# Kernel optimization log

Measured on AMD Instinct MI355X. Metric: run time of the kernel, lower is better.

Reference implementation:

```python
import jax, jax.numpy as jnp
import numpy as np

B, G, D, N_HEADS, FFN, L = 16, 2048, 256, 8, 1024, 4
HEAD_DIM = D // N_HEADS
EPS_LN = 1e-5
MASK_TOKEN = -10.0
REE_BASE = 100.0


def setup_inputs() -> dict:
    key = jax.random.key(0)
    ks = jax.random.split(key, 20)
    s = 0.02
    inp = {
        'x': jax.random.normal(ks[0], (B, G), jnp.float32),
        'gene_emb': jax.random.normal(ks[1], (G, D), jnp.float32) * s,
        'inv_freq': (1.0 / REE_BASE ** (jnp.arange(0, D, 2, dtype=jnp.float32) / D)),
        'Wq': jax.random.normal(ks[2], (L, D, D), jnp.float32) * s,
        'bq': jnp.zeros((L, D), jnp.float32),
        'Wk': jax.random.normal(ks[3], (L, D, D), jnp.float32) * s,
        'bk': jnp.zeros((L, D), jnp.float32),
        'Wv': jax.random.normal(ks[4], (L, D, D), jnp.float32) * s,
        'bv': jnp.zeros((L, D), jnp.float32),
        'ln1_g': jnp.ones((L, D), jnp.float32),
        'ln1_b': jnp.zeros((L, D), jnp.float32),
        'ln2_g': jnp.ones((L, D), jnp.float32),
        'ln2_b': jnp.zeros((L, D), jnp.float32),
        'WU': jax.random.normal(ks[5], (L, D, FFN), jnp.float32) * s,
        'bU': jnp.zeros((L, FFN), jnp.float32),
        'WV': jax.random.normal(ks[6], (L, FFN, D), jnp.float32) * s,
        'bV': jnp.zeros((L, D), jnp.float32),
        'Wout': jax.random.normal(ks[7], (D, 1), jnp.float32) * s,
        'bout': jnp.zeros((1,), jnp.float32),
    }
    return inp


def layernorm(x, g, b):
    m = x.mean(-1, keepdims=True)
    v = ((x - m) ** 2).mean(-1, keepdims=True)
    return (x - m) / jnp.sqrt(v + EPS_LN) * g + b


def causal_linear_attention(q, k, v):
    # q, k already feature-mapped ('sqr'); shapes [B, S, H, dh]
    b, s, h, dh = q.shape
    qs, ks_, vs = (jnp.moveaxis(t, 1, 0) for t in (q, k, v))  # [S,B,H,dh]
    num0 = jnp.zeros((b, h, dh, dh), q.dtype)
    den0 = jnp.zeros((b, h, dh), q.dtype)

    def step(carry, qkv):
        num_s, den_s = carry
        qt, kt, vt = qkv
        num_s = num_s + jnp.einsum('bhf,bhd->bhfd', kt, vt)
        den_s = den_s + kt
        num = jnp.einsum('bhf,bhfd->bhd', qt, num_s)
        den = jnp.einsum('bhf,bhf->bh', qt, den_s)
        return (num_s, den_s), num / (den[..., None] + 1e-16)

    _, out = jax.lax.scan(step, (num0, den0), (qs, ks_, vs))  # [S,B,H,dh]
    return jnp.moveaxis(out, 0, 1).reshape(b, s, h * dh)


def reference(x, gene_emb, inv_freq, Wq, bq, Wk, bk, Wv, bv,
              ln1_g, ln1_b, ln2_g, ln2_b, WU, bU, WV, bV, Wout, bout):
    b, g = x.shape
    # Rotary Expression Embedding
    freqs = x[..., None] * inv_freq  # [B,G,D/2]
    emb = jnp.concatenate([jnp.sin(freqs), jnp.cos(freqs)], axis=-1)  # [B,G,D]
    emb = jnp.where((x == MASK_TOKEN)[..., None], 0.0, emb)
    h = gene_emb[None] + emb  # [B,G,D]

    for l in range(Wq.shape[0]):
        hn = layernorm(h, ln1_g[l], ln1_b[l])  # pre-LN (on_gptln=True)
        q = (hn @ Wq[l] + bq[l]).reshape(b, g, N_HEADS, HEAD_DIM) ** 2
        k = (hn @ Wk[l] + bk[l]).reshape(b, g, N_HEADS, HEAD_DIM) ** 2
        v = (hn @ Wv[l] + bv[l]).reshape(b, g, N_HEADS, HEAD_DIM)
        h = h + causal_linear_attention(q, k, v)
        hn2 = layernorm(h, ln2_g[l], ln2_b[l])
        h = h + jax.nn.gelu(hn2 @ WU[l] + bU[l], approximate=False) @ WV[l] + bV[l]
    return (h @ Wout + bout).squeeze(-1)  # [B,G]
```

## Files before the change

kernel.cpp:

```cpp
#include <hip/hip_runtime.h>
#include <math.h>


#define GG 2048
#define DD 256
#define NROWS 32768
#define NC 32
#define CS 64

typedef __attribute__((ext_vector_type(8))) short bf16x8;
typedef __attribute__((ext_vector_type(4))) float f32x4;

struct FalseT { static constexpr bool value = false; };
struct TrueT  { static constexpr bool value = true;  };

__device__ __forceinline__ short f2bf(float f) {
  union { float f; unsigned u; } v; v.f = f;
  unsigned r = v.u + 0x7FFFu + ((v.u >> 16) & 1u);
  return (short)(r >> 16);
}
__device__ __forceinline__ float bf2f(short s) {
  union { unsigned u; float f; } v; v.u = ((unsigned)(unsigned short)s) << 16;
  return v.f;
}
__device__ __forceinline__ void gld16(const short* g, short* l) {
  __builtin_amdgcn_global_load_lds(
      (const __attribute__((address_space(1))) void*)g,
      (__attribute__((address_space(3))) void*)l, 16, 0, 0);
}
__device__ __forceinline__ float fast_gelu(float x) {
  float y = 1.595769122f * (x + 0.044715f * x * x * x);
  return x / (1.0f + __expf(-y));
}

__global__ __launch_bounds__(256) void embed_kernel(
    const float* __restrict__ x, const float* __restrict__ ge,
    const float* __restrict__ invf, float* __restrict__ h) {
  int bg = blockIdx.x * 4 + (threadIdx.x >> 6);
  int g = bg & (GG - 1);
  int lane = threadIdx.x & 63;
  float xv = x[bg];
  int d = lane * 4;
  float4 e;
  if (lane < 32) {
    float4 f = *(const float4*)&invf[d];
    e.x = sinf(xv * f.x); e.y = sinf(xv * f.y);
    e.z = sinf(xv * f.z); e.w = sinf(xv * f.w);
  } else {
    float4 f = *(const float4*)&invf[d - 128];
    e.x = cosf(xv * f.x); e.y = cosf(xv * f.y);
    e.z = cosf(xv * f.z); e.w = cosf(xv * f.w);
  }
  if (xv == -10.0f) { e.x = 0.f; e.y = 0.f; e.z = 0.f; e.w = 0.f; }
  float4 gv = *(const float4*)&ge[(size_t)g * DD + d];
  float4 o; o.x = gv.x + e.x; o.y = gv.y + e.y; o.z = gv.z + e.z; o.w = gv.w + e.w;
  *(float4*)&h[(size_t)bg * DD + d] = o;
}

__global__ __launch_bounds__(256) void ln_tiled(
    const float* __restrict__ h, const float* __restrict__ gamma,
    const float* __restrict__ beta, short* __restrict__ outT) {
  __shared__ float mean_s[32], rstd_s[32];
  __shared__ float gls[256], bls[256];
  int r0 = blockIdx.x * 32;
  int tid = threadIdx.x;
  gls[tid] = gamma[tid]; bls[tid] = beta[tid];
  {
    int row = tid >> 3, seg = tid & 7;
    const float4* hp = (const float4*)(h + (size_t)(r0 + row) * DD + seg * 32);
    float s = 0.f, s2 = 0.f;
#pragma unroll
    for (int i = 0; i < 8; ++i) {
      float4 v = hp[i];
      s += v.x + v.y + v.z + v.w;
      s2 += v.x * v.x + v.y * v.y + v.z * v.z + v.w * v.w;
    }
    s += __shfl_xor(s, 1); s += __shfl_xor(s, 2); s += __shfl_xor(s, 4);
    s2 += __shfl_xor(s2, 1); s2 += __shfl_xor(s2, 2); s2 += __shfl_xor(s2, 4);
    if (seg == 0) {
      float mn = s * (1.0f / 256.0f);
      mean_s[row] = mn;
      rstd_s[row] = rsqrtf(s2 * (1.0f / 256.0f) - mn * mn + 1e-5f);
    }
  }
  __syncthreads();
  int row = tid & 31, kc8 = (tid >> 5) & 3, half = tid >> 7;
  float mn = mean_s[row], rs = rstd_s[row];
  size_t hrow = (size_t)(r0 + row) * DD;
  int trow = (r0 & 127) + row;
  short* tb = outT + (size_t)(r0 >> 7) * 8 * 4096 + (kc8 * 128 + trow) * 8;
#pragma unroll
  for (int j = 0; j < 4; ++j) {
    int kb = half * 4 + j;
    int k0 = kb * 32 + kc8 * 8;
    float4 x0 = *(const float4*)&h[hrow + k0];
    float4 x1 = *(const float4*)&h[hrow + k0 + 4];
    float4 g0 = *(const float4*)&gls[k0], g1 = *(const float4*)&gls[k0 + 4];
    float4 b0 = *(const float4*)&bls[k0], b1 = *(const float4*)&bls[k0 + 4];
    bf16x8 aw;
    aw[0] = f2bf((x0.x - mn) * rs * g0.x + b0.x);
    aw[1] = f2bf((x0.y - mn) * rs * g0.y + b0.y);
    aw[2] = f2bf((x0.z - mn) * rs * g0.z + b0.z);
    aw[3] = f2bf((x0.w - mn) * rs * g0.w + b0.w);
    aw[4] = f2bf((x1.x - mn) * rs * g1.x + b1.x);
    aw[5] = f2bf((x1.y - mn) * rs * g1.y + b1.y);
    aw[6] = f2bf((x1.z - mn) * rs * g1.z + b1.z);
    aw[7] = f2bf((x1.w - mn) * rs * g1.w + b1.w);
    *(bf16x8*)&tb[(size_t)kb * 4096] = aw;
  }
}

__global__ __launch_bounds__(256) void prep_weights(
    const float* __restrict__ Wq, const float* __restrict__ Wk,
    const float* __restrict__ Wv, const float* __restrict__ WU,
    const float* __restrict__ WV,
    short* __restrict__ TQ, short* __restrict__ TK, short* __restrict__ TV,
    short* __restrict__ TU, short* __restrict__ TVd) {
  int zz = blockIdx.z, l = blockIdx.y;
  const float* src; short* dst; int Kd, Nd;
  if (zz == 0) { src = Wq; dst = TQ; Kd = 256; Nd = 256; }
  else if (zz == 1) { src = Wk; dst = TK; Kd = 256; Nd = 256; }
  else if (zz == 2) { src = Wv; dst = TV; Kd = 256; Nd = 256; }
  else if (zz == 3) { src = WU; dst = TU; Kd = 256; Nd = 1024; }
  else { src = WV; dst = TVd; Kd = 1024; Nd = 256; }
  int tot = Kd * Nd;
  int e = blockIdx.x * 256 + threadIdx.x;
  if (e >= tot) return;
  int t = e >> 12;
  int cslot = (e >> 3) & 511;
  int elem = e & 7;
  int kc8 = cslot >> 7, rn = cslot & 127;
  int nKb = Kd >> 5;
  int nt = t / nKb, kb = t - nt * nKb;
  int n = nt * 128 + rn, k = kb * 32 + kc8 * 8 + elem;
  dst[(size_t)l * tot + e] = f2bf(src[(size_t)l * tot + (size_t)k * Nd + n]);
}

template <int K, int EPI>
__global__ __launch_bounds__(256) void gemm_t(
    const short* __restrict__ A, const short* __restrict__ B0,
    const short* __restrict__ B1, const short* __restrict__ B2,
    const float* __restrict__ bias0, const float* __restrict__ bias1,
    const float* __restrict__ bias2,
    short* __restrict__ o0, short* __restrict__ o1, short* __restrict__ o2,
    float* __restrict__ outf, int N) {
  __shared__ __align__(16) short L[24576];
  constexpr int nIter = K / 32;
  int z = blockIdx.z;
  const short* Bt = (z == 0) ? B0 : (z == 1) ? B1 : B2;
  const float* bias = (z == 0) ? bias0 : (z == 1) ? bias1 : bias2;
  short* outz = (z == 0) ? o0 : (z == 1) ? o1 : o2;
  int m0 = blockIdx.x * 128, n0 = blockIdx.y * 128;
  int tid = threadIdx.x;
  int lane = tid & 63, w = tid >> 6;
  int q = lane >> 4, r = lane & 15;
  int wm = (w >> 1) * 64, wn = (w & 1) * 64;
  const short* At = A + (size_t)blockIdx.x * nIter * 4096;
  const short* Btl = Bt + (size_t)blockIdx.y * nIter * 4096;
  f32x4 vzero = {0.f, 0.f, 0.f, 0.f};
  f32x4 acc[4][4];
#pragma unroll
  for (int i = 0; i < 4; ++i)
#pragma unroll
    for (int j = 0; j < 4; ++j) acc[i][j] = vzero;

  int c0 = tid * 8, c1 = (tid + 256) * 8;
#pragma unroll
  for (int g = 0; g < 3; ++g) {
    gld16(At + g * 4096 + c0, &L[g * 4096 + c0]);
    gld16(At + g * 4096 + c1, &L[g * 4096 + c1]);
    gld16(Btl + g * 4096 + c0, &L[12288 + g * 4096 + c0]);
    gld16(Btl + g * 4096 + c1, &L[12288 + g * 4096 + c1]);
  }

  int abase = (q * 128 + wm + r) * 8;
  int bbase = (q * 128 + wn + r) * 8;

#pragma unroll
  for (int gi = 0; gi < nIter; ++gi) {
    const int rem = nIter - 1 - gi;
    if (rem >= 2)      __builtin_amdgcn_s_waitcnt(0x0f78);
    else if (rem == 1) __builtin_amdgcn_s_waitcnt(0x0f74);
    else               __builtin_amdgcn_s_waitcnt(0x0f70);
    __builtin_amdgcn_s_barrier();
    const int cur = gi % 3;
    const short* Asc = &L[cur * 4096];
    const short* Bsc = &L[12288 + cur * 4096];
    bf16x8 af[4], bfr[4];
#pragma unroll
    for (int mt = 0; mt < 4; ++mt)
      af[mt] = *(const bf16x8*)&Asc[abase + mt * 16 * 8];
#pragma unroll
    for (int nt = 0; nt < 4; ++nt)
      bfr[nt] = *(const bf16x8*)&Bsc[bbase + nt * 16 * 8];
#pragma unroll
    for (int mt = 0; mt < 4; ++mt)
#pragma unroll
      for (int nt = 0; nt < 4; ++nt)
        acc[mt][nt] = __builtin_amdgcn_mfma_f32_16x16x32_bf16(bfr[nt], af[mt], acc[mt][nt], 0, 0, 0);
    __builtin_amdgcn_s_waitcnt(0xc07f);
    __builtin_amdgcn_s_barrier();
    if (gi + 3 < nIter) {
      size_t kn = (size_t)(gi + 3) * 4096;
      gld16(At + kn + c0, &L[cur * 4096 + c0]);
      gld16(At + kn + c1, &L[cur * 4096 + c1]);
      gld16(Btl + kn + c0, &L[12288 + cur * 4096 + c0]);
      gld16(Btl + kn + c1, &L[12288 + cur * 4096 + c1]);
    }
  }

  float4 bias4[4];
#pragma unroll
  for (int nt = 0; nt < 4; ++nt) bias4[nt] = *(const float4*)&bias[n0 + wn + nt * 16 + q * 4];

  if (EPI == 0) {
    short* T = L;
#pragma unroll
    for (int mt = 0; mt < 4; ++mt) {
      int ml = wm + mt * 16 + r;
#pragma unroll
      for (int nt = 0; nt < 4; ++nt) {
        f32x4 v = acc[mt][nt];
        v[0] += bias4[nt].x; v[1] += bias4[nt].y; v[2] += bias4[nt].z; v[3] += bias4[nt].w;
        if (z < 2) { v[0] *= v[0]; v[1] *= v[1]; v[2] *= v[2]; v[3] *= v[3]; }
        short4 pk; pk.x = f2bf(v[0]); pk.y = f2bf(v[1]); pk.z = f2bf(v[2]); pk.w = f2bf(v[3]);
        *(short4*)&T[ml * 132 + wn + nt * 16 + q * 4] = pk;
      }
    }
    __syncthreads();
#pragma unroll
    for (int t2 = 0; t2 < 2; ++t2) {
      int task = tid + t2 * 256;
      int row = task & 127, hl = task >> 7;
      size_t obase = ((size_t)((n0 >> 5) + hl) * NROWS + m0 + row) * 32;
#pragma unroll
      for (int j = 0; j < 4; ++j)
        *(bf16x8*)&outz[obase + j * 8] = *(const bf16x8*)&T[row * 132 + hl * 32 + j * 8];
    }
  } else if (EPI == 1) {
#pragma unroll
    for (int mt = 0; mt < 4; ++mt) {
      int ml = wm + mt * 16 + r;
#pragma unroll
      for (int nt = 0; nt < 4; ++nt) {
        f32x4 v = acc[mt][nt];
        v[0] += bias4[nt].x; v[1] += bias4[nt].y; v[2] += bias4[nt].z; v[3] += bias4[nt].w;
#pragma unroll
        for (int e = 0; e < 4; ++e) v[e] = fast_gelu(v[e]);
        short4 o; o.x = f2bf(v[0]); o.y = f2bf(v[1]); o.z = f2bf(v[2]); o.w = f2bf(v[3]);
        int n = n0 + wn + nt * 16 + q * 4;
        size_t ti = ((size_t)blockIdx.x * (N >> 5) + (n >> 5)) * 4096 +
                    (size_t)(((n >> 3) & 3) << 10) + (ml << 3) + (n & 7);
        *(short4*)&outz[ti] = o;
      }
    }
  } else {
    float* TF = (float*)L;
#pragma unroll
    for (int half = 0; half < 2; ++half) {
      __syncthreads();
      if ((w & 1) == half) {
#pragma unroll
        for (int mt = 0; mt < 4; ++mt) {
          int ml = wm + mt * 16 + r;
#pragma unroll
          for (int nt = 0; nt < 4; ++nt) {
            f32x4 v = acc[mt][nt];
            v[0] += bias4[nt].x; v[1] += bias4[nt].y; v[2] += bias4[nt].z; v[3] += bias4[nt].w;
            *(f32x4*)&TF[ml * 68 + nt * 16 + q * 4] = v;
          }
        }
      }
      __syncthreads();
      int row = tid >> 1, col = (tid & 1) * 32;
      size_t hoff = (size_t)(m0 + row) * N + n0 + half * 64 + col;
#pragma unroll
      for (int j = 0; j < 8; ++j) {
        float4 add = *(const float4*)&TF[row * 68 + col + j * 4];
        float4 cur4 = *(float4*)&outf[hoff + j * 4];
        cur4.x += add.x; cur4.y += add.y; cur4.z += add.z; cur4.w += add.w;
        *(float4*)&outf[hoff + j * 4] = cur4;
      }
    }
  }
}

__global__ __launch_bounds__(512) void ffn_fused(
    const short* __restrict__ A, const short* __restrict__ TUw,
    const short* __restrict__ TVw, const float* __restrict__ bUp,
    const float* __restrict__ bVp, float* __restrict__ h) {
  __shared__ __align__(16) short L[75776];
  float* BU = (float*)&L[73728];
  int tid = threadIdx.x;
  int lane = tid & 63, w = tid >> 6;
  int q = lane >> 4, r = lane & 15;
  int wmU = (w >> 2) * 64, wnU = (w & 3) * 32;
  int wmD = (w >> 2) * 64, wnD = (w & 3) * 64;
  int c16 = tid * 8;
  const short* At = A + (size_t)blockIdx.x * 32768;

  if (tid < 256) *(float4*)&BU[tid * 4] = *(const float4*)&bUp[tid * 4];

#pragma unroll
  for (int i = 0; i < 8; ++i) gld16(At + i * 4096 + c16, &L[i * 4096 + c16]);

  auto issueUp = [&](int ss, int jj, int buf) {
    short* dst = &L[49152 + buf * 8192];
    const short* g0 = TUw + ((size_t)ss * 8 + jj * 2) * 4096;
    gld16(g0 + c16, dst + c16);
    gld16(g0 + 4096 + c16, dst + 4096 + c16);
  };
  auto issueDown = [&](int ss, int ii, int buf) {
    short* dst = &L[49152 + buf * 8192];
    gld16(TVw + (size_t)(ss * 4 + ii) * 4096 + c16, dst + c16);
    gld16(TVw + (size_t)(32 + ss * 4 + ii) * 4096 + c16, dst + 4096 + c16);
  };

  issueUp(0, 0, 0); issueUp(0, 1, 1); issueUp(0, 2, 2);

  f32x4 vzero = {0.f, 0.f, 0.f, 0.f};
  f32x4 accm[4][2], acco[4][4];
#pragma unroll
  for (int mt = 0; mt < 4; ++mt) {
#pragma unroll
    for (int nt = 0; nt < 2; ++nt) accm[mt][nt] = vzero;
#pragma unroll
    for (int nt = 0; nt < 4; ++nt) acco[mt][nt] = vzero;
  }

  int cur = 0;

  auto slice = [&](int s, auto lastc) {
    constexpr bool LAST = decltype(lastc)::value;
#pragma unroll
    for (int j = 0; j < 4; ++j) {
      __builtin_amdgcn_s_waitcnt(0x0f74);
      __builtin_amdgcn_s_barrier();
      const short* Ws = &L[49152 + cur * 8192];
#pragma unroll
      for (int kk = 0; kk < 2; ++kk) {
        int kb = j * 2 + kk;
        bf16x8 af[4], bfr[2];
#pragma unroll
        for (int mt = 0; mt < 4; ++mt)
          af[mt] = *(const bf16x8*)&L[kb * 4096 + (q * 128 + wmU + mt * 16 + r) * 8];
#pragma unroll
        for (int nt = 0; nt < 2; ++nt)
          bfr[nt] = *(const bf16x8*)&Ws[kk * 4096 + (q * 128 + wnU + nt * 16 + r) * 8];
#pragma unroll
        for (int mt = 0; mt < 4; ++mt)
#pragma unroll
          for (int nt = 0; nt < 2; ++nt)
            accm[mt][nt] = __builtin_amdgcn_mfma_f32_16x16x32_bf16(bfr[nt], af[mt], accm[mt][nt], 0, 0, 0);
      }
      if (j == 3) {
        float4 b4[2];
#pragma unroll
        for (int nt = 0; nt < 2; ++nt)
          b4[nt] = *(const float4*)&BU[s * 128 + wnU + nt * 16 + q * 4];
#pragma unroll
        for (int mt = 0; mt < 4; ++mt) {
          int row = wmU + mt * 16 + r;
#pragma unroll
          for (int nt = 0; nt < 2; ++nt) {
            f32x4 v = accm[mt][nt];
            v[0] += b4[nt].x; v[1] += b4[nt].y; v[2] += b4[nt].z; v[3] += b4[nt].w;
            short4 pk;
            pk.x = f2bf(fast_gelu(v[0])); pk.y = f2bf(fast_gelu(v[1]));
            pk.z = f2bf(fast_gelu(v[2])); pk.w = f2bf(fast_gelu(v[3]));
            int kc8 = 2 * nt + (q >> 1);
            *(short4*)&L[32768 + (w & 3) * 4096 + (kc8 * 128 + row) * 8 + (q & 1) * 4] = pk;
            accm[mt][nt] = vzero;
          }
        }
      }
      __builtin_amdgcn_s_waitcnt(0xc07f);
      __builtin_amdgcn_s_barrier();
      if (j == 0) issueUp(s, 3, cur);
      else issueDown(s, j - 1, cur);
      cur = (cur == 2) ? 0 : cur + 1;
    }
#pragma unroll
    for (int i = 0; i < 4; ++i) {
      if (LAST && i == 2)      __builtin_amdgcn_s_waitcnt(0x0f72);
      else if (LAST && i == 3) __builtin_amdgcn_s_waitcnt(0x0f70);
      else                     __builtin_amdgcn_s_waitcnt(0x0f74);
      __builtin_amdgcn_s_barrier();
      const short* Ws = &L[49152 + cur * 8192];
      bf16x8 am[4], bvf[4];
#pragma unroll
      for (int mt = 0; mt < 4; ++mt)
        am[mt] = *(const bf16x8*)&L[32768 + i * 4096 + (q * 128 + wmD + mt * 16 + r) * 8];
#pragma unroll
      for (int nt = 0; nt < 4; ++nt)
        bvf[nt] = *(const bf16x8*)&Ws[(wnD >> 7) * 4096 + (q * 128 + (wnD & 127) + nt * 16 + r) * 8];
#pragma unroll
      for (int mt = 0; mt < 4; ++mt)
#pragma unroll
        for (int nt = 0; nt < 4; ++nt)
          acco[mt][nt] = __builtin_amdgcn_mfma_f32_16x16x32_bf16(bvf[nt], am[mt], acco[mt][nt], 0, 0, 0);
      __builtin_amdgcn_s_waitcnt(0xc07f);
      __builtin_amdgcn_s_barrier();
      if (i == 0) issueDown(s, 3, cur);
      else if (!LAST) issueUp(s + 1, i - 1, cur);
      cur = (cur == 2) ? 0 : cur + 1;
    }
  };

  for (int s = 0; s < 7; ++s) slice(s, FalseT{});
  slice(7, TrueT{});

  float4 bv4[4];
#pragma unroll
  for (int nt = 0; nt < 4; ++nt) bv4[nt] = *(const float4*)&bVp[wnD + nt * 16 + q * 4];
  float* TF = (float*)L;
#pragma unroll
  for (int mt = 0; mt < 4; ++mt) {
    int row = wmD + mt * 16 + r;
#pragma unroll
    for (int nt = 0; nt < 4; ++nt) {
      f32x4 v = acco[mt][nt];
      v[0] += bv4[nt].x; v[1] += bv4[nt].y; v[2] += bv4[nt].z; v[3] += bv4[nt].w;
      *(f32x4*)&TF[row * 260 + wnD + nt * 16 + q * 4] = v;
    }
  }
  __syncthreads();
  size_t hbase = ((size_t)blockIdx.x * 128 + w * 16) * DD;
#pragma unroll
  for (int j = 0; j < 16; ++j) {
    float4 add = *(const float4*)&TF[(w * 16 + j) * 260 + lane * 4];
    float4 c4 = *(float4*)&h[hbase + (size_t)j * DD + lane * 4];
    c4.x += add.x; c4.y += add.y; c4.z += add.z; c4.w += add.w;
    *(float4*)&h[hbase + (size_t)j * DD + lane * 4] = c4;
  }
}

__global__ __launch_bounds__(256) void attn_chunk_kv(
    const short* __restrict__ Kb, const short* __restrict__ Vb,
    float* __restrict__ St, float* __restrict__ Zc) {
  __shared__ short Kt[4][32 * 72];
  __shared__ short Vt[4][32 * 72];
  int wid = threadIdx.x >> 6;
  int blk = blockIdx.x * 4 + wid;
  int c = blk & (NC - 1), bh = blk >> 5;
  int b = bh >> 3, hh = bh & 7;
  int lane = threadIdx.x & 63, q = lane >> 4, r = lane & 15;
  size_t rowbase = ((size_t)hh * NROWS + b * GG + c * CS + lane) * 32;
#pragma unroll
  for (int j = 0; j < 4; ++j) {
    bf16x8 kv = *(const bf16x8*)&Kb[rowbase + j * 8];
    bf16x8 vv = *(const bf16x8*)&Vb[rowbase + j * 8];
#pragma unroll
    for (int e = 0; e < 8; ++e) {
      Kt[wid][(j * 8 + e) * 72 + lane] = kv[e];
      Vt[wid][(j * 8 + e) * 72 + lane] = vv[e];
    }
  }
  __syncthreads();
  f32x4 vzero = {0.f, 0.f, 0.f, 0.f};
  f32x4 acc[2][2];
#pragma unroll
  for (int i = 0; i < 2; ++i)
#pragma unroll
    for (int j = 0; j < 2; ++j) acc[i][j] = vzero;
#pragma unroll
  for (int ks = 0; ks < 2; ++ks) {
    bf16x8 afr[2], bfr[2];
#pragma unroll
    for (int mt = 0; mt < 2; ++mt) afr[mt] = *(const bf16x8*)&Kt[wid][(mt * 16 + r) * 72 + ks * 32 + q * 8];
#pragma unroll
    for (int nt = 0; nt < 2; ++nt) bfr[nt] = *(const bf16x8*)&Vt[wid][(nt * 16 + r) * 72 + ks * 32 + q * 8];
#pragma unroll
    for (int mt = 0; mt < 2; ++mt)
#pragma unroll
      for (int nt = 0; nt < 2; ++nt)
        acc[mt][nt] = __builtin_amdgcn_mfma_f32_16x16x32_bf16(afr[mt], bfr[nt], acc[mt][nt], 0, 0, 0);
  }
  float* stp = St + ((size_t)bh * NC + c) * 1024;
#pragma unroll
  for (int mt = 0; mt < 2; ++mt)
#pragma unroll
    for (int nt = 0; nt < 2; ++nt)
      *(f32x4*)&stp[(nt * 16 + r) * 32 + mt * 16 + q * 4] = acc[mt][nt];
  if (lane < 32) {
    float s = 0.f;
#pragma unroll
    for (int j = 0; j < 8; ++j) {
      bf16x8 kr = *(const bf16x8*)&Kt[wid][lane * 72 + j * 8];
#pragma unroll
      for (int e = 0; e < 8; ++e) s += bf2f(kr[e]);
    }
    Zc[((size_t)bh * NC + c) * 32 + lane] = s;
  }
}

__global__ __launch_bounds__(1024) void attn_prefix(float* __restrict__ St, float* __restrict__ Zc) {
  int bh = blockIdx.x, i = threadIdx.x;
  float run = 0.f;
  float* p = St + (size_t)bh * NC * 1024 + i;
#pragma unroll
  for (int c = 0; c < NC; ++c) { float t = p[(size_t)c * 1024]; p[(size_t)c * 1024] = run; run += t; }
  if (i < 32) {
    float rz = 0.f;
    float* pz = Zc + (size_t)bh * NC * 32 + i;
#pragma unroll
    for (int c = 0; c < NC; ++c) { float t = pz[c * 32]; pz[c * 32] = rz; rz += t; }
  }
}

__global__ __launch_bounds__(256) void attn_intra(
    const short* __restrict__ Qb, const short* __restrict__ Kb,
    const short* __restrict__ Vb, const float* __restrict__ St,
    const float* __restrict__ Zc, float* __restrict__ h) {
  __shared__ short P[4][64 * 72];
  __shared__ short Vt[4][32 * 72];
  __shared__ float den[4][64];
  int wid = threadIdx.x >> 6;
  int blk = blockIdx.x * 4 + wid;
  int c = blk & (NC - 1), bh = blk >> 5;
  int b = bh >> 3, hh = bh & 7;
  int lane = threadIdx.x & 63, q = lane >> 4, r = lane & 15;
  size_t hrow0 = (size_t)b * GG + c * CS;
  size_t qrow0 = (size_t)hh * NROWS + b * GG + c * CS;

  const float* zp = Zc + ((size_t)bh * NC + c) * 32;
  float qz = 0.f;
  {
    size_t qoff = (qrow0 + lane) * 32;
#pragma unroll
    for (int j = 0; j < 4; ++j) {
      bf16x8 qv = *(const bf16x8*)&Qb[qoff + j * 8];
#pragma unroll
      for (int e = 0; e < 8; ++e) qz += bf2f(qv[e]) * zp[j * 8 + e];
    }
  }
  den[wid][lane] = qz;

  {
    size_t voff = (qrow0 + lane) * 32;
#pragma unroll
    for (int j = 0; j < 4; ++j) {
      bf16x8 vv = *(const bf16x8*)&Vb[voff + j * 8];
#pragma unroll
      for (int e = 0; e < 8; ++e) Vt[wid][(j * 8 + e) * 72 + lane] = vv[e];
    }
  }

  bf16x8 ak[4], bqf[4];
#pragma unroll
  for (int t4 = 0; t4 < 4; ++t4) {
    ak[t4]  = *(const bf16x8*)&Kb[(qrow0 + t4 * 16 + r) * 32 + q * 8];
    bqf[t4] = *(const bf16x8*)&Qb[(qrow0 + t4 * 16 + r) * 32 + q * 8];
  }
  f32x4 vzero = {0.f, 0.f, 0.f, 0.f};
  f32x4 pacc[4][4];
#pragma unroll
  for (int mt = 0; mt < 4; ++mt)
#pragma unroll
    for (int nt = 0; nt < 4; ++nt)
      pacc[mt][nt] = __builtin_amdgcn_mfma_f32_16x16x32_bf16(ak[mt], bqf[nt], vzero, 0, 0, 0);

  float rs[4] = {0.f, 0.f, 0.f, 0.f};
#pragma unroll
  for (int nt = 0; nt < 4; ++nt) {
    int t = nt * 16 + r;
#pragma unroll
    for (int mt = 0; mt < 4; ++mt) {
      short4 pk;
#pragma unroll
      for (int rr = 0; rr < 4; ++rr) {
        int s = mt * 16 + q * 4 + rr;
        float pv = (s <= t) ? pacc[mt][nt][rr] : 0.f;
        rs[nt] += pv;
        ((short*)&pk)[rr] = f2bf(pv);
      }
      *(short4*)&P[wid][t * 72 + mt * 16 + q * 4] = pk;
    }
  }
#pragma unroll
  for (int nt = 0; nt < 4; ++nt) {
    rs[nt] += __shfl_xor(rs[nt], 16);
    rs[nt] += __shfl_xor(rs[nt], 32);
  }
  __syncthreads();
  if (lane < 16) {
#pragma unroll
    for (int nt = 0; nt < 4; ++nt) den[wid][nt * 16 + lane] += rs[nt];
  }
  __syncthreads();

  f32x4 oacc[4][2];
#pragma unroll
  for (int mt = 0; mt < 4; ++mt)
#pragma unroll
    for (int nt2 = 0; nt2 < 2; ++nt2) oacc[mt][nt2] = vzero;
  const float* stp = St + ((size_t)bh * NC + c) * 1024;
#pragma unroll
  for (int nt2 = 0; nt2 < 2; ++nt2) {
    float4 s0 = *(const float4*)&stp[(nt2 * 16 + r) * 32 + q * 8];
    float4 s1 = *(const float4*)&stp[(nt2 * 16 + r) * 32 + q * 8 + 4];
    bf16x8 bs;
    bs[0] = f2bf(s0.x); bs[1] = f2bf(s0.y); bs[2] = f2bf(s0.z); bs[3] = f2bf(s0.w);
    bs[4] = f2bf(s1.x); bs[5] = f2bf(s1.y); bs[6] = f2bf(s1.z); bs[7] = f2bf(s1.w);
#pragma unroll
    for (int mt = 0; mt < 4; ++mt)
      oacc[mt][nt2] = __builtin_amdgcn_mfma_f32_16x16x32_bf16(bqf[mt], bs, oacc[mt][nt2], 0, 0, 0);
  }
#pragma unroll
  for (int ks = 0; ks < 2; ++ks) {
    bf16x8 ap[4];
#pragma unroll
    for (int mt = 0; mt < 4; ++mt)
      ap[mt] = *(const bf16x8*)&P[wid][(mt * 16 + r) * 72 + ks * 32 + q * 8];
#pragma unroll
    for (int nt2 = 0; nt2 < 2; ++nt2) {
      bf16x8 bv_ = *(const bf16x8*)&Vt[wid][(nt2 * 16 + r) * 72 + ks * 32 + q * 8];
#pragma unroll
      for (int mt = 0; mt < 4; ++mt)
        oacc[mt][nt2] = __builtin_amdgcn_mfma_f32_16x16x32_bf16(ap[mt], bv_, oacc[mt][nt2], 0, 0, 0);
    }
  }

#pragma unroll
  for (int mt = 0; mt < 4; ++mt) {
#pragma unroll
    for (int rr = 0; rr < 4; ++rr) {
      int t = mt * 16 + q * 4 + rr;
      float inv = 1.0f / (den[wid][t] + 1e-16f);
#pragma unroll
      for (int nt2 = 0; nt2 < 2; ++nt2) {
        int d = nt2 * 16 + r;
        size_t off = (hrow0 + t) * DD + hh * 32 + d;
        h[off] += oacc[mt][nt2][rr] * inv;
      }
    }
  }
}

__global__ __launch_bounds__(256) void out_proj(
    const float* __restrict__ h, const float* __restrict__ Wout,
    const float* __restrict__ bout, float* __restrict__ out) {
  int row = blockIdx.x * 4 + (threadIdx.x >> 6);
  int lane = threadIdx.x & 63;
  float4 a = *(const float4*)&h[(size_t)row * DD + lane * 4];
  float4 w = *(const float4*)&Wout[lane * 4];
  float s = a.x * w.x + a.y * w.y + a.z * w.z + a.w * w.w;
#pragma unroll
  for (int o = 1; o < 64; o <<= 1) s += __shfl_xor(s, o);
  if (lane == 0) out[row] = s + bout[0];
}

extern "C" void kernel_launch(void* const* d_in, const int* in_sizes, int n_in,
                              void* d_out, int out_size, void* d_ws, size_t ws_size,
                              hipStream_t stream) {
  const float* x    = (const float*)d_in[0];
  const float* ge   = (const float*)d_in[1];
  const float* invf = (const float*)d_in[2];
  const float* Wq   = (const float*)d_in[3];
  const float* bq   = (const float*)d_in[4];
  const float* Wk   = (const float*)d_in[5];
  const float* bk   = (const float*)d_in[6];
  const float* Wv   = (const float*)d_in[7];
  const float* bv   = (const float*)d_in[8];
  const float* ln1g = (const float*)d_in[9];
  const float* ln1b = (const float*)d_in[10];
  const float* ln2g = (const float*)d_in[11];
  const float* ln2b = (const float*)d_in[12];
  const float* WU   = (const float*)d_in[13];
  const float* bU   = (const float*)d_in[14];
  const float* WV   = (const float*)d_in[15];
  const float* bV   = (const float*)d_in[16];
  const float* Wout = (const float*)d_in[17];
  const float* bout = (const float*)d_in[18];
  float* out = (float*)d_out;

  char* ws = (char*)d_ws;
  float* h   = (float*)(ws + 0);
  short* hn  = (short*)(ws + 33554432);
  char*  R   = ws + 50331648;
  short* qb  = (short*)(R + 0);
  short* kb  = (short*)(R + 16777216);
  short* vb  = (short*)(R + 33554432);
  float* St  = (float*)(R + 50331648);
  float* Zc  = (float*)(R + 67108864);
  char*  WT  = R + 67633152;
  short* TQ  = (short*)(WT + 0);
  short* TK  = (short*)(WT + 524288);
  short* TVq = (short*)(WT + 1048576);
  short* TU  = (short*)(WT + 1572864);
  short* TVd = (short*)(WT + 3670016);

  prep_weights<<<dim3(1024, 4, 5), 256, 0, stream>>>(Wq, Wk, Wv, WU, WV, TQ, TK, TVq, TU, TVd);
  embed_kernel<<<NROWS / 4, 256, 0, stream>>>(x, ge, invf, h);

  for (int l = 0; l < 4; ++l) {
    ln_tiled<<<NROWS / 32, 256, 0, stream>>>(h, ln1g + l * 256, ln1b + l * 256, hn);
    gemm_t<256, 0><<<dim3(256, 2, 3), 256, 0, stream>>>(
        hn, TQ + l * 65536, TK + l * 65536, TVq + l * 65536,
        bq + l * 256, bk + l * 256, bv + l * 256,
        qb, kb, vb, nullptr, 256);
    attn_chunk_kv<<<1024, 256, 0, stream>>>(kb, vb, St, Zc);
    attn_prefix<<<128, 1024, 0, stream>>>(St, Zc);
    attn_intra<<<1024, 256, 0, stream>>>(qb, kb, vb, St, Zc, h);
    ln_tiled<<<NROWS / 32, 256, 0, stream>>>(h, ln2g + l * 256, ln2b + l * 256, hn);
    ffn_fused<<<256, 512, 0, stream>>>(hn, TU + l * 262144, TVd + l * 262144,
                                       bU + l * 1024, bV + l * 256, h);
  }
  out_proj<<<NROWS / 4, 256, 0, stream>>>(h, Wout, bout, out);
}
```

Baseline: 748.7 us.

## Restructure FFN weight streaming into double-buffered larger stages

Replaces the triple-buffered 8K-element weight ring in the fused FFN kernel with a double buffer of 16K-element stages. Each stage now covers four up-projection k-blocks or two down-projection k-blocks, which halves the number of barrier/wait points per slice. The up-projection bias is read straight from global memory into registers instead of being staged in LDS. LDS use grows to 160KB, and the prefetch depth drops from two stages ahead to one. That could expose more load latency or reduce occupancy.

After: 756.4 us. Within noise of the previous version (+1.0%).

```diff
diff --git a/kernel.cpp b/kernel.cpp
--- a/kernel.cpp
+++ b/kernel.cpp
@@ -289,34 +289,39 @@
     const short* __restrict__ A, const short* __restrict__ TUw,
     const short* __restrict__ TVw, const float* __restrict__ bUp,
     const float* __restrict__ bVp, float* __restrict__ h) {
-  __shared__ __align__(16) short L[75776];
-  float* BU = (float*)&L[73728];
+  __shared__ __align__(16) short L[81920];
   int tid = threadIdx.x;
   int lane = tid & 63, w = tid >> 6;
   int q = lane >> 4, r = lane & 15;
   int wmU = (w >> 2) * 64, wnU = (w & 3) * 32;
   int wmD = (w >> 2) * 64, wnD = (w & 3) * 64;
-  int c16 = tid * 8;
   const short* At = A + (size_t)blockIdx.x * 32768;
 
-  if (tid < 256) *(float4*)&BU[tid * 4] = *(const float4*)&bUp[tid * 4];
-
-#pragma unroll
-  for (int i = 0; i < 8; ++i) gld16(At + i * 4096 + c16, &L[i * 4096 + c16]);
-
-  auto issueUp = [&](int ss, int jj, int buf) {
-    short* dst = &L[49152 + buf * 8192];
-    const short* g0 = TUw + ((size_t)ss * 8 + jj * 2) * 4096;
-    gld16(g0 + c16, dst + c16);
-    gld16(g0 + 4096 + c16, dst + 4096 + c16);
+#pragma unroll
+  for (int i = 0; i < 8; ++i)
+    gld16(At + (i * 512 + tid) * 8, &L[(i * 512 + tid) * 8]);
+
+  auto issueFor = [&](int t) {
+    short* dst = &L[49152 + (t & 1) * 16384];
+    int ss = t >> 2, pp = t & 3;
+    if (pp < 2) {
+      const short* g0 = TUw + ((size_t)ss * 8 + pp * 4) * 4096;
+#pragma unroll
+      for (int i = 0; i < 4; ++i)
+        gld16(g0 + (i * 512 + tid) * 8, dst + (i * 512 + tid) * 8);
+    } else {
+      int kbg0 = ss * 4 + (pp - 2) * 2;
+#pragma unroll
+      for (int kl = 0; kl < 2; ++kl) {
+        gld16(TVw + (size_t)(kbg0 + kl) * 4096 + tid * 8,
+              dst + kl * 8192 + tid * 8);
+        gld16(TVw + (size_t)(32 + kbg0 + kl) * 4096 + tid * 8,
+              dst + kl * 8192 + 4096 + tid * 8);
+      }
+    }
   };
-  auto issueDown = [&](int ss, int ii, int buf) {
-    short* dst = &L[49152 + buf * 8192];
-    gld16(TVw + (size_t)(ss * 4 + ii) * 4096 + c16, dst + c16);
-    gld16(TVw + (size_t)(32 + ss * 4 + ii) * 4096 + c16, dst + 4096 + c16);
-  };
-
-  issueUp(0, 0, 0); issueUp(0, 1, 1); issueUp(0, 2, 2);
+
+  issueFor(0); issueFor(1);
 
   f32x4 vzero = {0.f, 0.f, 0.f, 0.f};
   f32x4 accm[4][2], acco[4][4];
@@ -327,44 +332,42 @@
 #pragma unroll
     for (int nt = 0; nt < 4; ++nt) acco[mt][nt] = vzero;
   }
-
-  int cur = 0;
+  float4 b4[2];
 
   auto slice = [&](int s, auto lastc) {
     constexpr bool LAST = decltype(lastc)::value;
 #pragma unroll
-    for (int j = 0; j < 4; ++j) {
+    for (int p = 0; p < 2; ++p) {
+      int sig = s * 4 + p;
       __builtin_amdgcn_s_waitcnt(0x0f74);
       __builtin_amdgcn_s_barrier();
-      const short* Ws = &L[49152 + cur * 8192];
-#pragma unroll
-      for (int kk = 0; kk < 2; ++kk) {
-        int kb = j * 2 + kk;
+      const short* Ws = &L[49152 + (sig & 1) * 16384];
+#pragma unroll
+      for (int kl = 0; kl < 4; ++kl) {
+        int kb = p * 4 + kl;
         bf16x8 af[4], bfr[2];
 #pragma unroll
         for (int mt = 0; mt < 4; ++mt)
           af[mt] = *(const bf16x8*)&L[kb * 4096 + (q * 128 + wmU + mt * 16 + r) * 8];
 #pragma unroll
         for (int nt = 0; nt < 2; ++nt)
-          bfr[nt] = *(const bf16x8*)&Ws[kk * 4096 + (q * 128 + wnU + nt * 16 + r) * 8];
+          bfr[nt] = *(const bf16x8*)&Ws[kl * 4096 + (q * 128 + wnU + nt * 16 + r) * 8];
 #pragma unroll
         for (int mt = 0; mt < 4; ++mt)
 #pragma unroll
           for (int nt = 0; nt < 2; ++nt)
-            accm[mt][nt] = __builtin_amdgcn_mfma_f32_16x16x32_bf16(bfr[nt], af[mt], accm[mt][nt], 0, 0, 0);
-      }
-      if (j == 3) {
-        float4 b4[2];
-#pragma unroll
-        for (int nt = 0; nt < 2; ++nt)
-          b4[nt] = *(const float4*)&BU[s * 128 + wnU + nt * 16 + q * 4];
+            accm[mt][nt] = __builtin_amdgcn_mfma_f32_16x16x32_bf16(
+                bfr[nt], af[mt], accm[mt][nt], 0, 0, 0);
+      }
+      if (p == 1) {
 #pragma unroll
         for (int mt = 0; mt < 4; ++mt) {
           int row = wmU + mt * 16 + r;
 #pragma unroll
           for (int nt = 0; nt < 2; ++nt) {
             f32x4 v = accm[mt][nt];
-            v[0] += b4[nt].x; v[1] += b4[nt].y; v[2] += b4[nt].z; v[3] += b4[nt].w;
+            float4 bb = b4[nt];
+            v[0] += bb.x; v[1] += bb.y; v[2] += bb.z; v[3] += bb.w;
             short4 pk;
             pk.x = f2bf(fast_gelu(v[0])); pk.y = f2bf(fast_gelu(v[1]));
             pk.z = f2bf(fast_gelu(v[2])); pk.w = f2bf(fast_gelu(v[3]));
@@ -376,34 +379,40 @@
       }
       __builtin_amdgcn_s_waitcnt(0xc07f);
       __builtin_amdgcn_s_barrier();
-      if (j == 0) issueUp(s, 3, cur);
-      else issueDown(s, j - 1, cur);
-      cur = (cur == 2) ? 0 : cur + 1;
-    }
-#pragma unroll
-    for (int i = 0; i < 4; ++i) {
-      if (LAST && i == 2)      __builtin_amdgcn_s_waitcnt(0x0f72);
-      else if (LAST && i == 3) __builtin_amdgcn_s_waitcnt(0x0f70);
-      else                     __builtin_amdgcn_s_waitcnt(0x0f74);
+      if (p == 0) {
+        b4[0] = *(const float4*)&bUp[s * 128 + wnU + q * 4];
+        b4[1] = *(const float4*)&bUp[s * 128 + wnU + 16 + q * 4];
+      }
+      if (sig + 2 < 32) issueFor(sig + 2);
+    }
+#pragma unroll
+    for (int p2 = 0; p2 < 2; ++p2) {
+      int sig = s * 4 + 2 + p2;
+      if (LAST && p2 == 1) __builtin_amdgcn_s_waitcnt(0x0f70);
+      else                 __builtin_amdgcn_s_waitcnt(0x0f74);
       __builtin_amdgcn_s_barrier();
-      const short* Ws = &L[49152 + cur * 8192];
-      bf16x8 am[4], bvf[4];
-#pragma unroll
-      for (int mt = 0; mt < 4; ++mt)
-        am[mt] = *(const bf16x8*)&L[32768 + i * 4096 + (q * 128 + wmD + mt * 16 + r) * 8];
-#pragma unroll
-      for (int nt = 0; nt < 4; ++nt)
-        bvf[nt] = *(const bf16x8*)&Ws[(wnD >> 7) * 4096 + (q * 128 + (wnD & 127) + nt * 16 + r) * 8];
-#pragma unroll
-      for (int mt = 0; mt < 4; ++mt)
+      const short* Ws = &L[49152 + (sig & 1) * 16384];
+#pragma unroll
+      for (int kl = 0; kl < 2; ++kl) {
+        int mtile = p2 * 2 + kl;
+        bf16x8 am[4], bvf[4];
+#pragma unroll
+        for (int mt = 0; mt < 4; ++mt)
+          am[mt] = *(const bf16x8*)&L[32768 + mtile * 4096 + (q * 128 + wmD + mt * 16 + r) * 8];
 #pragma unroll
         for (int nt = 0; nt < 4; ++nt)
-          acco[mt][nt] = __builtin_amdgcn_mfma_f32_16x16x32_bf16(bvf[nt], am[mt], acco[mt][nt], 0, 0, 0);
+          bvf[nt] = *(const bf16x8*)&Ws[kl * 8192 + (wnD >> 7) * 4096 +
+                                        (q * 128 + (wnD & 127) + nt * 16 + r) * 8];
+#pragma unroll
+        for (int mt = 0; mt < 4; ++mt)
+#pragma unroll
+          for (int nt = 0; nt < 4; ++nt)
+            acco[mt][nt] = __builtin_amdgcn_mfma_f32_16x16x32_bf16(
+                bvf[nt], am[mt], acco[mt][nt], 0, 0, 0);
+      }
       __builtin_amdgcn_s_waitcnt(0xc07f);
       __builtin_amdgcn_s_barrier();
-      if (i == 0) issueDown(s, 3, cur);
-      else if (!LAST) issueUp(s + 1, i - 1, cur);
-      cur = (cur == 2) ? 0 : cur + 1;
+      if (sig + 2 < 32) issueFor(sig + 2);
     }
   };
 
```
